# Performance work log

Hardware: AMD Instinct MI355X
Metric: run time of the kernel (lower is better)

The kernel has to match this reference:

```python
import jax, jax.numpy as jnp
import numpy as np

D_MODEL, D_FFN, N_EXPERTS, TOP_K = 1024, 4096, 8, 2
BATCH, SEQ = 4, 1024


def setup_inputs() -> dict:
    key = jax.random.key(0)
    kx, kr, k1, k2, k3 = jax.random.split(key, 5)
    scale = 0.02
    return {
        "x": jax.random.normal(kx, (BATCH, SEQ, D_MODEL), dtype=jnp.float32),
        "w_router": jax.random.normal(kr, (D_MODEL, N_EXPERTS), dtype=jnp.float32) * scale,
        "w1": jax.random.normal(k1, (N_EXPERTS, D_MODEL, D_FFN), dtype=jnp.float32) * scale,
        "w2": jax.random.normal(k2, (N_EXPERTS, D_FFN, D_MODEL), dtype=jnp.float32) * scale,
        "w3": jax.random.normal(k3, (N_EXPERTS, D_MODEL, D_FFN), dtype=jnp.float32) * scale,
    }


def reference(x, w_router, w1, w2, w3):
    B, S, D = x.shape
    E = w_router.shape[1]
    T = B * S
    xf = x.reshape(T, D)

    # --- router: softmax over experts, top-k, renormalize ---
    router_probs = jax.nn.softmax(xf @ w_router, axis=-1)          # (T, E)
    topk_probs, topk_idx = jax.lax.top_k(router_probs, TOP_K)      # (T, K)
    topk_probs = topk_probs / topk_probs.sum(axis=-1, keepdims=True)

    # per-token combine weight for each expert (top_k indices are distinct,
    # matching the torch per-slot accumulation exactly)
    comb = jnp.zeros((T, E), dtype=xf.dtype)
    comb = comb.at[jnp.arange(T)[:, None], topk_idx].add(topk_probs)  # (T, E)

    # --- dense SwiGLU experts (same math as masked loop) ---
    h = jnp.einsum("td,edf->tef", xf, w1)                          # (T, E, F)
    g = jnp.einsum("td,edf->tef", xf, w3)                          # (T, E, F)
    y = jnp.einsum("tef,efd->ted", jax.nn.silu(h) * g, w2)         # (T, E, D)
    out = jnp.einsum("te,ted->td", comb, y).reshape(B, S, D)

    # --- load-balance aux loss ---
    expert_mask = jax.nn.one_hot(topk_idx, E, dtype=jnp.float32).sum(axis=1)  # (T, E)
    tokens_per_expert = expert_mask.sum(axis=0) / T
    mean_probs = router_probs.mean(axis=0)
    aux_loss = E * jnp.sum(tokens_per_expert * mean_probs)
    return out, aux_loss
```

## Files before the change

### kernel.cpp

```cpp
#include <hip/hip_runtime.h>
#include <hip/hip_bf16.h>
#include <cstdint>
#include <cstddef>

#define TT 4096
#define DM 1024
#define DF 4096
#define NE 8
#define BTAB 72

typedef __attribute__((ext_vector_type(8))) short bf16x8;
typedef __attribute__((ext_vector_type(8))) unsigned short ushort8;
typedef __attribute__((ext_vector_type(4))) float f32x4;

static __device__ __forceinline__ unsigned short f2bf(float f) {
    union { float f; unsigned int u; } v; v.f = f;
    unsigned int u = v.u;
    return (unsigned short)((u + 0x7FFFu + ((u >> 16) & 1u)) >> 16);
}
static __device__ __forceinline__ float bf2f(unsigned short h) {
    union { unsigned int u; float f; } v; v.u = ((unsigned int)h) << 16;
    return v.f;
}

#define GLOAD16(gsrc, ldst)                                                        \
    __builtin_amdgcn_global_load_lds(                                              \
        (const __attribute__((address_space(1))) void*)(gsrc),                     \
        (__attribute__((address_space(3))) void*)(ldst), 16, 0, 0)

__global__ void transpose_to_bf16(const float* __restrict__ in,
                                  unsigned short* __restrict__ out,
                                  int R, int C) {
    __shared__ float tile[32][33];
    const int e = blockIdx.z;
    const float* src = in + (size_t)e * R * C;
    unsigned short* dst = out + (size_t)e * R * C;
    const int c0 = blockIdx.x * 32, r0 = blockIdx.y * 32;
    const int tx = threadIdx.x, ty = threadIdx.y;
    #pragma unroll
    for (int i = 0; i < 4; ++i) {
        int r = r0 + ty + i * 8;
        tile[ty + i * 8][tx] = src[(size_t)r * C + c0 + tx];
    }
    __syncthreads();
    #pragma unroll
    for (int i = 0; i < 4; ++i) {
        int c = c0 + ty + i * 8;
        dst[(size_t)c * R + r0 + tx] = f2bf(tile[tx][ty + i * 8]);
    }
}

__global__ void router_kernel(const float* __restrict__ x,
                              const float* __restrict__ wr,
                              unsigned short* __restrict__ xb,
                              int* __restrict__ topi, float* __restrict__ topw,
                              float* __restrict__ probsum) {
    __shared__ float s_ps[NE];
    const int tid = threadIdx.x;
    if (tid < NE) s_ps[tid] = 0.f;
    __syncthreads();
    const int wid = tid >> 6, lane = tid & 63;
    const int t = blockIdx.x * 4 + wid;
    float acc[NE] = {0.f, 0.f, 0.f, 0.f, 0.f, 0.f, 0.f, 0.f};
    const float* xr = x + (size_t)t * DM;
    unsigned short* xbr = xb + (size_t)t * DM;
    for (int it = 0; it < DM / 64; ++it) {
        int d = it * 64 + lane;
        float xv = xr[d];
        xbr[d] = f2bf(xv);
        const float* w = wr + d * NE;
        #pragma unroll
        for (int e = 0; e < NE; ++e) acc[e] = fmaf(xv, w[e], acc[e]);
    }
    #pragma unroll
    for (int e = 0; e < NE; ++e) {
        float v = acc[e];
        #pragma unroll
        for (int off = 32; off; off >>= 1) v += __shfl_xor(v, off);
        acc[e] = v;
    }
    if (lane == 0) {
        float m = acc[0];
        #pragma unroll
        for (int e = 1; e < NE; ++e) m = fmaxf(m, acc[e]);
        float p[NE], s = 0.f;
        #pragma unroll
        for (int e = 0; e < NE; ++e) { p[e] = expf(acc[e] - m); s += p[e]; }
        float inv = 1.f / s;
        #pragma unroll
        for (int e = 0; e < NE; ++e) { p[e] *= inv; atomicAdd(&s_ps[e], p[e]); }
        int i1 = 0; float p1 = p[0];
        #pragma unroll
        for (int e = 1; e < NE; ++e) if (p[e] > p1) { p1 = p[e]; i1 = e; }
        int i2 = -1; float p2 = -1.f;
        #pragma unroll
        for (int e = 0; e < NE; ++e) if (e != i1 && p[e] > p2) { p2 = p[e]; i2 = e; }
        float rs = 1.f / (p1 + p2);
        topi[t * 2] = i1; topi[t * 2 + 1] = i2;
        topw[t * 2] = p1 * rs; topw[t * 2 + 1] = p2 * rs;
    }
    __syncthreads();
    if (tid < NE) atomicAdd(&probsum[tid], s_ps[tid]);
}

__global__ void assign_kernel(const int* __restrict__ topi,
                              int* __restrict__ list, int* __restrict__ slotpos,
                              int* __restrict__ cnt) {
    const int e = blockIdx.x;
    __shared__ int s_wc[4];
    const int tid = threadIdx.x, wid = tid >> 6, lane = tid & 63;
    int running = 0;
    for (int base = 0; base < TT; base += 256) {
        int t = base + tid;
        int hit = 0, slot = 0;
        int a = topi[2 * t], b = topi[2 * t + 1];
        if (a == e) { hit = 1; slot = 0; }
        else if (b == e) { hit = 1; slot = 1; }
        unsigned long long m = __ballot(hit);
        if (lane == 0) s_wc[wid] = __popcll(m);
        __syncthreads();
        int pre = 0, tot = 0;
        #pragma unroll
        for (int q = 0; q < 4; ++q) { int c = s_wc[q]; tot += c; if (q < wid) pre += c; }
        if (hit) {
            int pos = running + pre + __popcll(m & ((1ull << lane) - 1ull));
            list[e * TT + pos] = t;
            slotpos[2 * t + slot] = pos;
        }
        running += tot;
        __syncthreads();
    }
    if (tid == 0) cnt[e] = running;
}

__global__ void finalize_kernel(const int* __restrict__ cnt,
                                const float* __restrict__ probsum,
                                int* __restrict__ offs,
                                unsigned int* __restrict__ blocktab,
                                float* __restrict__ out_aux) {
    int o = 0;
    float aux = 0.f;
    int nb = 0;
    for (int e = 0; e < NE; ++e) {
        offs[e] = o; o += cnt[e];
        aux += (float)cnt[e] * probsum[e];
        int nrb = (cnt[e] + 127) >> 7;
        for (int rb = 0; rb < nrb; ++rb) blocktab[nb++] = ((unsigned)e << 16) | rb;
    }
    while (nb < BTAB) blocktab[nb++] = 0xFFFFFFFFu;
    *out_aux = (float)NE * aux / ((float)TT * (float)TT);
}

static __device__ __forceinline__ const bf16x8* frag_ptr(
        const unsigned short* base, int row, int ph16) {
    return (const bf16x8*)((const char*)base + row * 64 + ph16);
}

__global__ __launch_bounds__(256, 2) void gemm1_kernel(
    const unsigned short* __restrict__ xb,
    const unsigned short* __restrict__ w1T,
    const unsigned short* __restrict__ w3T,
    unsigned short* __restrict__ act,
    const int* __restrict__ list,
    const int* __restrict__ cnt,
    const int* __restrict__ offs,
    const unsigned int* __restrict__ blocktab) {
    const unsigned int tab = blocktab[blockIdx.y];
    if (tab == 0xFFFFFFFFu) return;
    const int e = tab >> 16;
    const int rowbase = (int)(tab & 0xFFFFu) << 7;
    const int ce = cnt[e];
    const int fbase = blockIdx.x * 128;

    __shared__ __align__(16) unsigned short As[128 * 32];
    __shared__ __align__(16) unsigned short B1s[128 * 32];
    __shared__ __align__(16) unsigned short B3s[128 * 32];

    const int tid = threadIdx.x;
    const int lrow = tid >> 2;
    const int q = (tid & 3) ^ ((tid >> 3) & 3);

    int sp0 = rowbase + lrow;       if (sp0 >= ce) sp0 = ce - 1;
    int sp1 = rowbase + 64 + lrow;  if (sp1 >= ce) sp1 = ce - 1;
    const size_t tok0 = (size_t)list[e * TT + sp0];
    const size_t tok1 = (size_t)list[e * TT + sp1];

    const unsigned short* a0 = xb + tok0 * DM + q * 8;
    const unsigned short* a1 = xb + tok1 * DM + q * 8;
    const unsigned short* b1a = w1T + ((size_t)e * DF + fbase + lrow) * DM + q * 8;
    const unsigned short* b1b = b1a + (size_t)64 * DM;
    const unsigned short* b3a = w3T + ((size_t)e * DF + fbase + lrow) * DM + q * 8;
    const unsigned short* b3b = b3a + (size_t)64 * DM;

    char* ldsA  = (char*)As  + tid * 16;
    char* ldsB1 = (char*)B1s + tid * 16;
    char* ldsB3 = (char*)B3s + tid * 16;

    const int wid = tid >> 6, lane = tid & 63;
    const int wm = wid >> 1, wn = wid & 1;
    const int g = lane >> 4, r = lane & 15;
    const int ph16 = (g ^ ((r >> 1) & 3)) << 4;

    f32x4 acch[4][4] = {};
    f32x4 accg[4][4] = {};

    for (int k0 = 0; k0 < DM; k0 += 32) {
        GLOAD16(a0 + k0,  ldsA);
        GLOAD16(a1 + k0,  ldsA + 4096);
        GLOAD16(b1a + k0, ldsB1);
        GLOAD16(b1b + k0, ldsB1 + 4096);
        GLOAD16(b3a + k0, ldsB3);
        GLOAD16(b3b + k0, ldsB3 + 4096);
        __syncthreads();
        bf16x8 af[4];
        #pragma unroll
        for (int m = 0; m < 4; ++m)
            af[m] = *frag_ptr(As, wm * 64 + m * 16 + r, ph16);
        #pragma unroll
        for (int n = 0; n < 4; ++n) {
            bf16x8 f1 = *frag_ptr(B1s, wn * 64 + n * 16 + r, ph16);
            bf16x8 f3 = *frag_ptr(B3s, wn * 64 + n * 16 + r, ph16);
            #pragma unroll
            for (int m = 0; m < 4; ++m) {
                acch[m][n] = __builtin_amdgcn_mfma_f32_16x16x32_bf16(af[m], f1, acch[m][n], 0, 0, 0);
                accg[m][n] = __builtin_amdgcn_mfma_f32_16x16x32_bf16(af[m], f3, accg[m][n], 0, 0, 0);
            }
        }
        __syncthreads();
    }

    const int ob = offs[e];
    #pragma unroll
    for (int m = 0; m < 4; ++m) {
        #pragma unroll
        for (int j = 0; j < 4; ++j) {
            const int pos = rowbase + wm * 64 + m * 16 + g * 4 + j;
            if (pos < ce) {
                unsigned short* arow = act + (size_t)(ob + pos) * DF + fbase + wn * 64;
                #pragma unroll
                for (int n = 0; n < 4; ++n) {
                    float h = acch[m][n][j];
                    float gv = accg[m][n][j];
                    float a = (h / (1.f + __expf(-h))) * gv;
                    arow[n * 16 + r] = f2bf(a);
                }
            }
        }
    }
}

__global__ __launch_bounds__(256, 2) void gemm2_kernel(
    const unsigned short* __restrict__ act,
    const unsigned short* __restrict__ w2T,
    unsigned short* __restrict__ ybuf,
    const int* __restrict__ cnt,
    const int* __restrict__ offs,
    const unsigned int* __restrict__ blocktab) {
    const unsigned int tab = blocktab[blockIdx.y];
    if (tab == 0xFFFFFFFFu) return;
    const int e = tab >> 16;
    const int rowbase = (int)(tab & 0xFFFFu) << 7;
    const int ce = cnt[e];
    const int dbase = blockIdx.x * 128;
    const int ob = offs[e];

    __shared__ __align__(16) unsigned short As[128 * 32];
    __shared__ __align__(16) unsigned short Bs[128 * 32];

    const int tid = threadIdx.x;
    const int lrow = tid >> 2;
    const int q = (tid & 3) ^ ((tid >> 3) & 3);

    int sp0 = rowbase + lrow;       if (sp0 >= ce) sp0 = ce - 1;
    int sp1 = rowbase + 64 + lrow;  if (sp1 >= ce) sp1 = ce - 1;

    const unsigned short* a0 = act + (size_t)(ob + sp0) * DF + q * 8;
    const unsigned short* a1 = act + (size_t)(ob + sp1) * DF + q * 8;
    const unsigned short* b0 = w2T + ((size_t)e * DM + dbase + lrow) * DF + q * 8;
    const unsigned short* b1 = b0 + (size_t)64 * DF;

    char* ldsA = (char*)As + tid * 16;
    char* ldsB = (char*)Bs + tid * 16;

    const int wid = tid >> 6, lane = tid & 63;
    const int wm = wid >> 1, wn = wid & 1;
    const int g = lane >> 4, r = lane & 15;
    const int ph16 = (g ^ ((r >> 1) & 3)) << 4;

    f32x4 acc[4][4] = {};

    for (int k0 = 0; k0 < DF; k0 += 32) {
        GLOAD16(a0 + k0, ldsA);
        GLOAD16(a1 + k0, ldsA + 4096);
        GLOAD16(b0 + k0, ldsB);
        GLOAD16(b1 + k0, ldsB + 4096);
        __syncthreads();
        bf16x8 af[4];
        #pragma unroll
        for (int m = 0; m < 4; ++m)
            af[m] = *frag_ptr(As, wm * 64 + m * 16 + r, ph16);
        #pragma unroll
        for (int n = 0; n < 4; ++n) {
            bf16x8 bfr = *frag_ptr(Bs, wn * 64 + n * 16 + r, ph16);
            #pragma unroll
            for (int m = 0; m < 4; ++m)
                acc[m][n] = __builtin_amdgcn_mfma_f32_16x16x32_bf16(af[m], bfr, acc[m][n], 0, 0, 0);
        }
        __syncthreads();
    }

    #pragma unroll
    for (int m = 0; m < 4; ++m) {
        #pragma unroll
        for (int j = 0; j < 4; ++j) {
            const int pos = rowbase + wm * 64 + m * 16 + g * 4 + j;
            if (pos < ce) {
                unsigned short* yrow = ybuf + (size_t)(ob + pos) * DM + dbase + wn * 64;
                #pragma unroll
                for (int n = 0; n < 4; ++n)
                    yrow[n * 16 + r] = f2bf(acc[m][n][j]);
            }
        }
    }
}

__global__ void combine_kernel(const unsigned short* __restrict__ ybuf,
                               const int* __restrict__ topi,
                               const float* __restrict__ topw,
                               const int* __restrict__ slotpos,
                               const int* __restrict__ offs,
                               float* __restrict__ out) {
    const int t = blockIdx.x;
    const int tid = threadIdx.x;
    const int e0 = topi[2 * t], e1 = topi[2 * t + 1];
    const int r0 = offs[e0] + slotpos[2 * t];
    const int r1 = offs[e1] + slotpos[2 * t + 1];
    const float w0 = topw[2 * t], w1 = topw[2 * t + 1];
    ushort4 a = *(const ushort4*)(ybuf + (size_t)r0 * DM + tid * 4);
    ushort4 b = *(const ushort4*)(ybuf + (size_t)r1 * DM + tid * 4);
    float4 o;
    o.x = w0 * bf2f(a.x) + w1 * bf2f(b.x);
    o.y = w0 * bf2f(a.y) + w1 * bf2f(b.y);
    o.z = w0 * bf2f(a.z) + w1 * bf2f(b.z);
    o.w = w0 * bf2f(a.w) + w1 * bf2f(b.w);
    *(float4*)(out + (size_t)t * DM + tid * 4) = o;
}

extern "C" void kernel_launch(void* const* d_in, const int* in_sizes, int n_in,
                              void* d_out, int out_size, void* d_ws, size_t ws_size,
                              hipStream_t stream) {
    (void)in_sizes; (void)n_in; (void)ws_size;
    const float* x  = (const float*)d_in[0];
    const float* wr = (const float*)d_in[1];
    const float* w1 = (const float*)d_in[2];
    const float* w2 = (const float*)d_in[3];
    const float* w3 = (const float*)d_in[4];
    float* out = (float*)d_out;

    char* ws = (char*)d_ws;
    size_t off = 0;
    auto alloc = [&](size_t bytes) -> void* {
        void* p = ws + off;
        off = (off + bytes + 255) & ~(size_t)255;
        return p;
    };
    unsigned short* w1T = (unsigned short*)alloc((size_t)NE * DF * DM * 2);
    unsigned short* w3T = (unsigned short*)alloc((size_t)NE * DF * DM * 2);
    unsigned short* w2T = (unsigned short*)alloc((size_t)NE * DM * DF * 2);
    unsigned short* act = (unsigned short*)alloc((size_t)2 * TT * DF * 2);
    unsigned short* xb  = (unsigned short*)alloc((size_t)TT * DM * 2);
    int*   topi    = (int*)alloc(TT * 2 * sizeof(int));
    float* topw    = (float*)alloc(TT * 2 * sizeof(float));
    int*   list    = (int*)alloc((size_t)NE * TT * sizeof(int));
    int*   slotpos = (int*)alloc(TT * 2 * sizeof(int));
    int*   cnt     = (int*)alloc(NE * sizeof(int));
    int*   offs    = (int*)alloc(NE * sizeof(int));
    float* probsum = (float*)alloc(NE * sizeof(float));
    unsigned int* blocktab = (unsigned int*)alloc(BTAB * sizeof(unsigned int));
    unsigned short* ybuf = w1T;

    hipMemsetAsync(probsum, 0, NE * sizeof(float), stream);

    dim3 tb(32, 8);
    transpose_to_bf16<<<dim3(DF / 32, DM / 32, NE), tb, 0, stream>>>(w1, w1T, DM, DF);
    transpose_to_bf16<<<dim3(DF / 32, DM / 32, NE), tb, 0, stream>>>(w3, w3T, DM, DF);
    transpose_to_bf16<<<dim3(DM / 32, DF / 32, NE), tb, 0, stream>>>(w2, w2T, DF, DM);

    router_kernel<<<TT / 4, 256, 0, stream>>>(x, wr, xb, topi, topw, probsum);
    assign_kernel<<<NE, 256, 0, stream>>>(topi, list, slotpos, cnt);
    finalize_kernel<<<1, 1, 0, stream>>>(cnt, probsum, offs, blocktab, out + (out_size - 1));

    gemm1_kernel<<<dim3(DF / 128, BTAB), 256, 0, stream>>>(xb, w1T, w3T, act, list, cnt, offs, blocktab);
    gemm2_kernel<<<dim3(DM / 128, BTAB), 256, 0, stream>>>(act, w2T, ybuf, cnt, offs, blocktab);
    combine_kernel<<<TT, 256, 0, stream>>>(ybuf, topi, topw, slotpos, offs, out);
}
```

Measured before the change: 481.4 us.

## Double-buffer LDS tiles in expert GEMMs and merge w1/w3 transposes

```diff
diff --git a/kernel.cpp b/kernel.cpp
--- a/kernel.cpp
+++ b/kernel.cpp
@@ -28,25 +28,48 @@
         (const __attribute__((address_space(1))) void*)(gsrc),                     \
         (__attribute__((address_space(3))) void*)(ldst), 16, 0, 0)
 
-__global__ void transpose_to_bf16(const float* __restrict__ in,
-                                  unsigned short* __restrict__ out,
-                                  int R, int C) {
+__global__ void transpose13_kernel(const float* __restrict__ w1,
+                                   const float* __restrict__ w3,
+                                   unsigned short* __restrict__ w1T,
+                                   unsigned short* __restrict__ w3T) {
+    __shared__ float tile[32][33];
+    const int z = blockIdx.z;
+    const int e = z & 7;
+    const float* src = (z < 8 ? w1 : w3) + (size_t)e * DM * DF;
+    unsigned short* dst = (z < 8 ? w1T : w3T) + (size_t)e * DM * DF;
+    const int c0 = blockIdx.x * 32, r0 = blockIdx.y * 32;
+    const int tx = threadIdx.x, ty = threadIdx.y;
+    #pragma unroll
+    for (int i = 0; i < 4; ++i) {
+        int r = r0 + ty + i * 8;
+        tile[ty + i * 8][tx] = src[(size_t)r * DF + c0 + tx];
+    }
+    __syncthreads();
+    #pragma unroll
+    for (int i = 0; i < 4; ++i) {
+        int c = c0 + ty + i * 8;
+        dst[(size_t)c * DM + r0 + tx] = f2bf(tile[tx][ty + i * 8]);
+    }
+}
+
+__global__ void transpose2_kernel(const float* __restrict__ in,
+                                  unsigned short* __restrict__ out) {
     __shared__ float tile[32][33];
     const int e = blockIdx.z;
-    const float* src = in + (size_t)e * R * C;
-    unsigned short* dst = out + (size_t)e * R * C;
+    const float* src = in + (size_t)e * DF * DM;
+    unsigned short* dst = out + (size_t)e * DF * DM;
     const int c0 = blockIdx.x * 32, r0 = blockIdx.y * 32;
     const int tx = threadIdx.x, ty = threadIdx.y;
     #pragma unroll
     for (int i = 0; i < 4; ++i) {
         int r = r0 + ty + i * 8;
-        tile[ty + i * 8][tx] = src[(size_t)r * C + c0 + tx];
+        tile[ty + i * 8][tx] = src[(size_t)r * DM + c0 + tx];
     }
     __syncthreads();
     #pragma unroll
     for (int i = 0; i < 4; ++i) {
         int c = c0 + ty + i * 8;
-        dst[(size_t)c * R + r0 + tx] = f2bf(tile[tx][ty + i * 8]);
+        dst[(size_t)c * DF + r0 + tx] = f2bf(tile[tx][ty + i * 8]);
     }
 }
 
@@ -172,9 +195,9 @@
     const int ce = cnt[e];
     const int fbase = blockIdx.x * 128;
 
-    __shared__ __align__(16) unsigned short As[128 * 32];
-    __shared__ __align__(16) unsigned short B1s[128 * 32];
-    __shared__ __align__(16) unsigned short B3s[128 * 32];
+    __shared__ __align__(16) unsigned short As[2 * 128 * 32];
+    __shared__ __align__(16) unsigned short B1s[2 * 128 * 32];
+    __shared__ __align__(16) unsigned short B3s[2 * 128 * 32];
 
     const int tid = threadIdx.x;
     const int lrow = tid >> 2;
@@ -204,30 +227,48 @@
     f32x4 acch[4][4] = {};
     f32x4 accg[4][4] = {};
 
-    for (int k0 = 0; k0 < DM; k0 += 32) {
-        GLOAD16(a0 + k0,  ldsA);
-        GLOAD16(a1 + k0,  ldsA + 4096);
-        GLOAD16(b1a + k0, ldsB1);
-        GLOAD16(b1b + k0, ldsB1 + 4096);
-        GLOAD16(b3a + k0, ldsB3);
-        GLOAD16(b3b + k0, ldsB3 + 4096);
-        __syncthreads();
+#define STAGE1(T, BUF)                                   \
+    {   const int koff = (T) * 32;                       \
+        const int bo = (BUF) * 8192;                     \
+        GLOAD16(a0 + koff,  ldsA + bo);                  \
+        GLOAD16(a1 + koff,  ldsA + bo + 4096);           \
+        GLOAD16(b1a + koff, ldsB1 + bo);                 \
+        GLOAD16(b1b + koff, ldsB1 + bo + 4096);          \
+        GLOAD16(b3a + koff, ldsB3 + bo);                 \
+        GLOAD16(b3b + koff, ldsB3 + bo + 4096); }
+
+    const int NT = DM / 32;
+    STAGE1(0, 0);
+    asm volatile("s_waitcnt vmcnt(0)" ::: "memory");
+    __builtin_amdgcn_s_barrier();
+    __builtin_amdgcn_sched_barrier(0);
+
+    for (int t = 0; t < NT; ++t) {
+        const int cur = t & 1;
+        if (t + 1 < NT) STAGE1(t + 1, cur ^ 1);
+        const unsigned short* Ac  = As  + cur * 4096;
+        const unsigned short* B1c = B1s + cur * 4096;
+        const unsigned short* B3c = B3s + cur * 4096;
         bf16x8 af[4];
         #pragma unroll
         for (int m = 0; m < 4; ++m)
-            af[m] = *frag_ptr(As, wm * 64 + m * 16 + r, ph16);
+            af[m] = *frag_ptr(Ac, wm * 64 + m * 16 + r, ph16);
         #pragma unroll
         for (int n = 0; n < 4; ++n) {
-            bf16x8 f1 = *frag_ptr(B1s, wn * 64 + n * 16 + r, ph16);
-            bf16x8 f3 = *frag_ptr(B3s, wn * 64 + n * 16 + r, ph16);
+            bf16x8 f1 = *frag_ptr(B1c, wn * 64 + n * 16 + r, ph16);
+            bf16x8 f3 = *frag_ptr(B3c, wn * 64 + n * 16 + r, ph16);
             #pragma unroll
             for (int m = 0; m < 4; ++m) {
                 acch[m][n] = __builtin_amdgcn_mfma_f32_16x16x32_bf16(af[m], f1, acch[m][n], 0, 0, 0);
                 accg[m][n] = __builtin_amdgcn_mfma_f32_16x16x32_bf16(af[m], f3, accg[m][n], 0, 0, 0);
             }
         }
-        __syncthreads();
-    }
+        __builtin_amdgcn_sched_barrier(0);
+        asm volatile("s_waitcnt vmcnt(0)" ::: "memory");
+        __builtin_amdgcn_s_barrier();
+        __builtin_amdgcn_sched_barrier(0);
+    }
+#undef STAGE1
 
     const int ob = offs[e];
     #pragma unroll
@@ -264,8 +305,8 @@
     const int dbase = blockIdx.x * 128;
     const int ob = offs[e];
 
-    __shared__ __align__(16) unsigned short As[128 * 32];
-    __shared__ __align__(16) unsigned short Bs[128 * 32];
+    __shared__ __align__(16) unsigned short As[2 * 128 * 32];
+    __shared__ __align__(16) unsigned short Bs[2 * 128 * 32];
 
     const int tid = threadIdx.x;
     const int lrow = tid >> 2;
@@ -289,25 +330,42 @@
 
     f32x4 acc[4][4] = {};
 
-    for (int k0 = 0; k0 < DF; k0 += 32) {
-        GLOAD16(a0 + k0, ldsA);
-        GLOAD16(a1 + k0, ldsA + 4096);
-        GLOAD16(b0 + k0, ldsB);
-        GLOAD16(b1 + k0, ldsB + 4096);
-        __syncthreads();
+#define STAGE2(T, BUF)                                   \
+    {   const int koff = (T) * 32;                       \
+        const int bo = (BUF) * 8192;                     \
+        GLOAD16(a0 + koff, ldsA + bo);                   \
+        GLOAD16(a1 + koff, ldsA + bo + 4096);            \
+        GLOAD16(b0 + koff, ldsB + bo);                   \
+        GLOAD16(b1 + koff, ldsB + bo + 4096); }
+
+    const int NT = DF / 32;
+    STAGE2(0, 0);
+    asm volatile("s_waitcnt vmcnt(0)" ::: "memory");
+    __builtin_amdgcn_s_barrier();
+    __builtin_amdgcn_sched_barrier(0);
+
+    for (int t = 0; t < NT; ++t) {
+        const int cur = t & 1;
+        if (t + 1 < NT) STAGE2(t + 1, cur ^ 1);
+        const unsigned short* Ac = As + cur * 4096;
+        const unsigned short* Bc = Bs + cur * 4096;
         bf16x8 af[4];
         #pragma unroll
         for (int m = 0; m < 4; ++m)
-            af[m] = *frag_ptr(As, wm * 64 + m * 16 + r, ph16);
+            af[m] = *frag_ptr(Ac, wm * 64 + m * 16 + r, ph16);
         #pragma unroll
         for (int n = 0; n < 4; ++n) {
-            bf16x8 bfr = *frag_ptr(Bs, wn * 64 + n * 16 + r, ph16);
+            bf16x8 bfr = *frag_ptr(Bc, wn * 64 + n * 16 + r, ph16);
             #pragma unroll
             for (int m = 0; m < 4; ++m)
                 acc[m][n] = __builtin_amdgcn_mfma_f32_16x16x32_bf16(af[m], bfr, acc[m][n], 0, 0, 0);
         }
-        __syncthreads();
-    }
+        __builtin_amdgcn_sched_barrier(0);
+        asm volatile("s_waitcnt vmcnt(0)" ::: "memory");
+        __builtin_amdgcn_s_barrier();
+        __builtin_amdgcn_sched_barrier(0);
+    }
+#undef STAGE2
 
     #pragma unroll
     for (int m = 0; m < 4; ++m) {
@@ -382,9 +440,8 @@
     hipMemsetAsync(probsum, 0, NE * sizeof(float), stream);
 
     dim3 tb(32, 8);
-    transpose_to_bf16<<<dim3(DF / 32, DM / 32, NE), tb, 0, stream>>>(w1, w1T, DM, DF);
-    transpose_to_bf16<<<dim3(DF / 32, DM / 32, NE), tb, 0, stream>>>(w3, w3T, DM, DF);
-    transpose_to_bf16<<<dim3(DM / 32, DF / 32, NE), tb, 0, stream>>>(w2, w2T, DF, DM);
+    transpose13_kernel<<<dim3(DF / 32, DM / 32, 2 * NE), tb, 0, stream>>>(w1, w3, w1T, w3T);
+    transpose2_kernel<<<dim3(DM / 32, DF / 32, NE), tb, 0, stream>>>(w2, w2T);
 
     router_kernel<<<TT / 4, 256, 0, stream>>>(x, wr, xb, topi, topw, probsum);
     assign_kernel<<<NE, 256, 0, stream>>>(topi, list, slotpos, cnt);
```

Result: no change. 480.6 us (-0.2%).
